# Performance work log

Measured on AMD Instinct MI355X. Metric: run time of the kernel, lower is better.

Reference implementation:

```python
import jax, jax.numpy as jnp
import numpy as np

B, A, G = 16, 32, 512      # batch, atoms, g_feat_in
S, M = 1024, 8             # subset samples, peaks per subset
E, OH = 5, 20              # element types, thermometer size per element
FE = E * OH                # formula encoding = 100
D = 512                    # internal_d
NBINS = 512                # spect bins
EPS = 1e-4


def _ln(x, g, b):
    m = x.mean(-1, keepdims=True)
    v = jnp.mean((x - m) ** 2, -1, keepdims=True)
    return (x - m) * jax.lax.rsqrt(v + 1e-5) * g + b


def setup_inputs() -> dict:
    key = jax.random.key(0)
    ks = jax.random.split(key, 16)
    vert_feat_in = jax.random.normal(ks[0], (B, A, G), jnp.float32)
    vert_mask_in = jnp.ones((B, A), jnp.float32)
    elem = jax.random.randint(ks[1], (B, A), 0, E)
    vert_element_oh = jax.nn.one_hot(elem, E, dtype=jnp.float32)
    atom_subsets = jax.random.randint(ks[2], (B, S, A), 0, 2).astype(jnp.int32)
    atom_subsets_peaks_mass_idx = jax.random.randint(ks[3], (B, S, M), 0, NBINS).astype(jnp.int32)
    atom_subsets_peaks_intensity = jax.random.uniform(ks[4], (B, S, M), jnp.float32)

    def lin(k, o, i):
        s = 1.0 / np.sqrt(i)
        return jax.random.uniform(k, (o, i), jnp.float32, -s, s)

    return dict(
        vert_feat_in=vert_feat_in, vert_mask_in=vert_mask_in,
        vert_element_oh=vert_element_oh, atom_subsets=atom_subsets,
        atom_subsets_peaks_mass_idx=atom_subsets_peaks_mass_idx,
        atom_subsets_peaks_intensity=atom_subsets_peaks_intensity,
        ln_sub_g=jnp.ones((G,)), ln_sub_b=jnp.zeros((G,)),
        W_ih=lin(ks[5], 3 * G, FE), W_hh=lin(ks[6], 3 * G, G),
        b_ih=jnp.zeros((3 * G,)), b_hh=jnp.zeros((3 * G,)),
        ln_post_g=jnp.ones((G,)), ln_post_b=jnp.zeros((G,)),
        W1=lin(ks[7], D, G), b1=jnp.zeros((D,)),
        W2a=lin(ks[8], D, D), b2a=jnp.zeros((D,)),
        W2b=lin(ks[9], D, D), b2b=jnp.zeros((D,)),
        ln_pre_g=jnp.ones((D,)), ln_pre_b=jnp.zeros((D,)),
        W_s=lin(ks[10], 1, D), b_s=jnp.zeros((1,)),
    )


def reference(vert_feat_in, vert_mask_in, vert_element_oh, atom_subsets,
              atom_subsets_peaks_mass_idx, atom_subsets_peaks_intensity,
              ln_sub_g, ln_sub_b, W_ih, W_hh, b_ih, b_hh,
              ln_post_g, ln_post_b, W1, b1, W2a, b2a, W2b, b2b,
              ln_pre_g, ln_pre_b, W_s, b_s):
    subs_f = atom_subsets.astype(jnp.float32)
    masked_vert = vert_feat_in * vert_mask_in[:, :, None]          # B,A,G
    subs_masked = subs_f * vert_mask_in[:, None, :]                 # B,S,A
    # subset-weighted pooling of vertex features
    swv_sum = jnp.einsum('baf,bsa->bsf', masked_vert, subs_masked)  # B,S,G
    subset_size = subs_masked.sum(-1) + EPS                         # B,S
    swv_mean = swv_sum / subset_size[..., None]
    h = _ln(swv_mean, ln_sub_g, ln_sub_b)                           # B,S,G
    # formula counts -> thermometer (accumulating) one-hot; .byte() cast kills grads
    counts = jax.lax.stop_gradient(
        jnp.einsum('bae,bsa->bse', vert_element_oh, subs_f))        # B,S,E
    therm = (jnp.arange(OH, dtype=jnp.float32)[None, None, None, :] < counts[..., None])
    formulae = therm.astype(jnp.float32).reshape(counts.shape[0], counts.shape[1], FE)
    # GRUCell: input=formula encoding, hidden=subset_normed
    gi = jnp.einsum('bsf,gf->bsg', formulae, W_ih) + b_ih           # B,S,3G
    gh = jnp.einsum('bsh,gh->bsg', h, W_hh) + b_hh
    gi_r, gi_z, gi_n = jnp.split(gi, 3, axis=-1)
    gh_r, gh_z, gh_n = jnp.split(gh, 3, axis=-1)
    r = jax.nn.sigmoid(gi_r + gh_r)
    z = jax.nn.sigmoid(gi_z + gh_z)
    n = jnp.tanh(gi_n + r * gh_n)
    combined = (1.0 - z) * n + z * h                                # B,S,G
    x = _ln(combined, ln_post_g, ln_post_b)
    x = jax.nn.relu(jnp.einsum('bsg,dg->bsd', x, W1) + b1)
    x = jax.nn.relu(jnp.einsum('bsd,ed->bse', x, W2a) + b2a)
    x = jax.nn.relu(jnp.einsum('bsd,ed->bse', x, W2b) + b2b)
    x = _ln(x, ln_pre_g, ln_pre_b)
    scores = (jnp.einsum('bsd,od->bso', x, W_s) + b_s)[..., 0]      # B,S
    probs = jax.nn.softmax(scores, axis=-1)                         # B,S
    # sparse mass-matrix multiply: scatter subset probs into spectrum bins
    weighted = atom_subsets_peaks_intensity * probs[:, :, None]     # B,S,M
    bidx = jnp.arange(probs.shape[0])[:, None, None]
    spect_out = jnp.zeros((probs.shape[0], NBINS), probs.dtype)
    spect_out = spect_out.at[bidx, atom_subsets_peaks_mass_idx].add(weighted)
    return spect_out, probs
```

## Files before the change

kernel.cpp:

```cpp
#include <hip/hip_runtime.h>

#define NB 16
#define NA 32
#define NG 512
#define NS 1024
#define NM 8
#define NE 5
#define NOH 20
#define NFE 100
#define NFEP 128
#define ND 512
#define NBINS 512
#define NTOK (NB * NS)

typedef unsigned short ushort_t;
typedef __attribute__((ext_vector_type(8))) short bf16x8;
typedef __attribute__((ext_vector_type(4))) float f32x4;

__device__ __forceinline__ ushort_t f2bf(float x) {
  union { float f; unsigned u; } v; v.f = x;
  unsigned r = v.u + 0x7FFF + ((v.u >> 16) & 1);
  return (ushort_t)(r >> 16);
}
__device__ __forceinline__ float bf2f(ushort_t b) {
  union { unsigned u; float f; } v; v.u = ((unsigned)b) << 16;
  return v.f;
}

__device__ __forceinline__ void gload_lds16(const void* g, void* l) {
  __builtin_amdgcn_global_load_lds(
      (const __attribute__((address_space(1))) void*)g,
      (__attribute__((address_space(3))) void*)l, 16, 0, 0);
}

__device__ inline float breduce256(float v, float* s) {
#pragma unroll
  for (int off = 32; off > 0; off >>= 1) v += __shfl_down(v, off);
  __syncthreads();
  if ((threadIdx.x & 63) == 0) s[threadIdx.x >> 6] = v;
  __syncthreads();
  return s[0] + s[1] + s[2] + s[3];
}

__global__ __launch_bounds__(256) void setup_kernel(
    const float* __restrict__ vert, const float* __restrict__ mask,
    const float* __restrict__ eloh, const int* __restrict__ subs,
    const float* __restrict__ Wih, const float* __restrict__ Whh,
    const float* __restrict__ W1, const float* __restrict__ W2a,
    const float* __restrict__ W2b,
    float* __restrict__ tcd,
    ushort_t* __restrict__ o_ih, ushort_t* __restrict__ o_hh,
    ushort_t* __restrict__ o1, ushort_t* __restrict__ o2a,
    ushort_t* __restrict__ o2b,
    ushort_t* __restrict__ VmT, ushort_t* __restrict__ S_bf) {
  int i = blockIdx.x * 256 + threadIdx.x;
  if (i < NTOK) {
    int b = i >> 10;
    const int* srow = subs + (size_t)i * NA;
    float cnt[NE] = {0.f, 0.f, 0.f, 0.f, 0.f};
    float z = 0.f;
    for (int a = 0; a < NA; a++) {
      float sb = (float)srow[a];
      z += sb * mask[b * NA + a];
      const float* eo = eloh + (size_t)(b * NA + a) * NE;
#pragma unroll
      for (int e = 0; e < NE; e++) cnt[e] += eo[e] * sb;
    }
    float* o = tcd + (size_t)i * 8;
#pragma unroll
    for (int e = 0; e < NE; e++) o[e] = cnt[e];
    o[5] = 1.0f / (z + 1e-4f);
    return;
  }
  i -= NTOK;
  if (i < 1536 * NFEP) {
    int r = i >> 7, c = i & 127;
    o_ih[i] = (c < NFE) ? f2bf(Wih[r * NFE + c]) : (ushort_t)0;
    return;
  }
  i -= 1536 * NFEP;
  if (i < 1536 * NG) { o_hh[i] = f2bf(Whh[i]); return; }
  i -= 1536 * NG;
  if (i < ND * NG) { o1[i] = f2bf(W1[i]); return; }
  i -= ND * NG;
  if (i < ND * ND) { o2a[i] = f2bf(W2a[i]); return; }
  i -= ND * ND;
  if (i < ND * ND) { o2b[i] = f2bf(W2b[i]); return; }
  i -= ND * ND;
  const int nV = NB * NG * NA;
  if (i < nV) {
    int b = i / (NG * NA); int rem = i % (NG * NA);
    int f = rem >> 5, a = rem & 31;
    float mk = mask[b * NA + a];
    VmT[i] = f2bf(vert[(size_t)b * NA * NG + a * NG + f] * mk * mk);
    return;
  }
  i -= nV;
  if (i < NTOK * NA) S_bf[i] = f2bf((float)subs[i]);
}

__global__ __launch_bounds__(256) void pool_gemm(
    const ushort_t* __restrict__ S_bf, const ushort_t* __restrict__ VmT,
    const float* __restrict__ tcd, float* __restrict__ SWV, int tok0) {
  __shared__ ushort_t As[128 * 32];
  __shared__ ushort_t Bs[128 * 32];
  const int t = threadIdx.x;
  const int w = t >> 6, lane = t & 63;
  const int wr = w >> 1, wc = w & 1;
  const int bm = blockIdx.x * 128;
  const int bn = blockIdx.y * 128;
  const int b = (tok0 + bm) >> 10;
  const int srow = lane >> 2, scol = (lane & 3) * 8;
  const ushort_t* Bbase = VmT + (size_t)b * NG * NA;
  gload_lds16(S_bf + (size_t)(tok0 + bm + w * 16 + srow) * 32 + scol, &As[w * 512]);
  gload_lds16(S_bf + (size_t)(tok0 + bm + 64 + w * 16 + srow) * 32 + scol, &As[2048 + w * 512]);
  gload_lds16(Bbase + (size_t)(bn + w * 16 + srow) * 32 + scol, &Bs[w * 512]);
  gload_lds16(Bbase + (size_t)(bn + 64 + w * 16 + srow) * 32 + scol, &Bs[2048 + w * 512]);
  __syncthreads();

  const int lr = lane & 15, lq = lane >> 4;
  f32x4 acc[4][4];
#pragma unroll
  for (int m = 0; m < 4; m++)
#pragma unroll
    for (int n = 0; n < 4; n++) acc[m][n] = (f32x4)0.f;
  bf16x8 a[4], bb[4];
#pragma unroll
  for (int m = 0; m < 4; m++)
    a[m] = *(const bf16x8*)&As[(wr * 64 + m * 16 + lr) * 32 + lq * 8];
#pragma unroll
  for (int n = 0; n < 4; n++)
    bb[n] = *(const bf16x8*)&Bs[(wc * 64 + n * 16 + lr) * 32 + lq * 8];
#pragma unroll
  for (int m = 0; m < 4; m++)
#pragma unroll
    for (int n = 0; n < 4; n++)
      acc[m][n] = __builtin_amdgcn_mfma_f32_16x16x32_bf16(a[m], bb[n], acc[m][n], 0, 0, 0);

#pragma unroll
  for (int n = 0; n < 4; n++) {
    const int col = bn + wc * 64 + n * 16 + lr;
#pragma unroll
    for (int m = 0; m < 4; m++) {
      f32x4 v = acc[m][n];
#pragma unroll
      for (int r = 0; r < 4; r++) {
        int row = bm + wr * 64 + m * 16 + lq * 4 + r;
        float inv = tcd[(size_t)(tok0 + row) * 8 + 5];
        SWV[(size_t)row * NG + col] = v[r] * inv;
      }
    }
  }
}

__global__ __launch_bounds__(256) void finish_kernel(
    const float* __restrict__ SWV, const float* __restrict__ tcd,
    const float* __restrict__ lng, const float* __restrict__ lnb,
    ushort_t* __restrict__ Hb, ushort_t* __restrict__ F, int tok0) {
  const int ltok = blockIdx.x;
  const int token = tok0 + ltok;
  const int t = threadIdx.x;
  __shared__ float s_red[4];
  float2 v = *(const float2*)&SWV[(size_t)ltok * NG + 2 * t];
  float mean = breduce256(v.x + v.y, s_red) * (1.0f / NG);
  float d0 = v.x - mean, d1 = v.y - mean;
  float var = breduce256(d0 * d0 + d1 * d1, s_red) * (1.0f / NG);
  float rstd = rsqrtf(var + 1e-5f);
  float2 g = *(const float2*)&lng[2 * t];
  float2 be = *(const float2*)&lnb[2 * t];
  ushort2 ho;
  ho.x = f2bf(d0 * rstd * g.x + be.x);
  ho.y = f2bf(d1 * rstd * g.y + be.y);
  *(ushort2*)&Hb[(size_t)ltok * NG + 2 * t] = ho;
  if (t < NFEP) {
    float vF = 0.f;
    if (t < NFE) {
      int e = t / NOH, o = t % NOH;
      vF = ((float)o < tcd[(size_t)token * 8 + e]) ? 1.0f : 0.0f;
    }
    F[(size_t)ltok * NFEP + t] = f2bf(vF);
  }
}

__global__ __launch_bounds__(256) void gemm_bf16(
    const ushort_t* __restrict__ A, const ushort_t* __restrict__ W,
    const float* __restrict__ bias, ushort_t* __restrict__ C,
    int K, int Dout, int mode) {
  __shared__ ushort_t As[2][4096];
  __shared__ ushort_t Bs[2][4096];
  const int t = threadIdx.x;
  const int w = t >> 6;
  const int lane = t & 63;
  const int wr = w >> 1, wc = w & 1;
  const int bm = blockIdx.x * 128, bn = blockIdx.y * 128;

  const int srow = lane >> 2;
  const int scol = (lane & 3) * 8;
  const ushort_t* Ag0 = A + (size_t)(bm + w * 16 + srow) * K + scol;
  const ushort_t* Ag1 = A + (size_t)(bm + 64 + w * 16 + srow) * K + scol;
  const ushort_t* Wg0 = W + (size_t)(bn + w * 16 + srow) * K + scol;
  const ushort_t* Wg1 = W + (size_t)(bn + 64 + w * 16 + srow) * K + scol;
  const int l0 = w * 512;
  const int l1 = 2048 + w * 512;

  const int lr = lane & 15;
  const int lq = lane >> 4;

  f32x4 acc[4][4];
#pragma unroll
  for (int m = 0; m < 4; m++)
#pragma unroll
    for (int n = 0; n < 4; n++) acc[m][n] = (f32x4)0.f;

  gload_lds16(Ag0, &As[0][l0]);
  gload_lds16(Ag1, &As[0][l1]);
  gload_lds16(Wg0, &Bs[0][l0]);
  gload_lds16(Wg1, &Bs[0][l1]);
  __syncthreads();

  const int nk = K >> 5;
  int cur = 0;
  for (int kt = 0; kt < nk; kt++) {
    if (kt + 1 < nk) {
      const int k1 = (kt + 1) << 5;
      gload_lds16(Ag0 + k1, &As[cur ^ 1][l0]);
      gload_lds16(Ag1 + k1, &As[cur ^ 1][l1]);
      gload_lds16(Wg0 + k1, &Bs[cur ^ 1][l0]);
      gload_lds16(Wg1 + k1, &Bs[cur ^ 1][l1]);
    }
    bf16x8 a[4], b[4];
#pragma unroll
    for (int m = 0; m < 4; m++)
      a[m] = *(const bf16x8*)&As[cur][(wr * 64 + m * 16 + lr) * 32 + lq * 8];
#pragma unroll
    for (int n = 0; n < 4; n++)
      b[n] = *(const bf16x8*)&Bs[cur][(wc * 64 + n * 16 + lr) * 32 + lq * 8];
#pragma unroll
    for (int m = 0; m < 4; m++)
#pragma unroll
      for (int n = 0; n < 4; n++)
        acc[m][n] = __builtin_amdgcn_mfma_f32_16x16x32_bf16(a[m], b[n], acc[m][n], 0, 0, 0);
    __syncthreads();
    cur ^= 1;
  }

#pragma unroll
  for (int n = 0; n < 4; n++) {
    const int col = bn + wc * 64 + n * 16 + lr;
    const float bv = bias[col];
#pragma unroll
    for (int m = 0; m < 4; m++) {
      f32x4 v = acc[m][n];
#pragma unroll
      for (int r = 0; r < 4; r++) {
        int row = bm + wr * 64 + m * 16 + lq * 4 + r;
        float u = v[r] + bv;
        if (mode == 1) u = fmaxf(u, 0.f);
        C[(size_t)row * Dout + col] = f2bf(u);
      }
    }
  }
}

__global__ __launch_bounds__(256) void gate_ln_kernel(
    const ushort_t* __restrict__ Gi, const ushort_t* __restrict__ Gh,
    const ushort_t* __restrict__ Hb, const float* __restrict__ lng,
    const float* __restrict__ lnb, ushort_t* __restrict__ X0) {
  const int token = blockIdx.x;
  const int t = threadIdx.x;
  __shared__ float s_red[4];
  const ushort_t* gi = Gi + (size_t)token * 1536;
  const ushort_t* gh = Gh + (size_t)token * 1536;
  ushort2 gir = *(const ushort2*)&gi[2 * t];
  ushort2 giz = *(const ushort2*)&gi[NG + 2 * t];
  ushort2 gin = *(const ushort2*)&gi[2 * NG + 2 * t];
  ushort2 ghr = *(const ushort2*)&gh[2 * t];
  ushort2 ghz = *(const ushort2*)&gh[NG + 2 * t];
  ushort2 ghn = *(const ushort2*)&gh[2 * NG + 2 * t];
  ushort2 hh = *(const ushort2*)&Hb[(size_t)token * NG + 2 * t];
  float c[2];
  {
    float r0 = 1.f / (1.f + expf(-(bf2f(gir.x) + bf2f(ghr.x))));
    float z0 = 1.f / (1.f + expf(-(bf2f(giz.x) + bf2f(ghz.x))));
    float n0 = tanhf(bf2f(gin.x) + r0 * bf2f(ghn.x));
    c[0] = (1.f - z0) * n0 + z0 * bf2f(hh.x);
    float r1 = 1.f / (1.f + expf(-(bf2f(gir.y) + bf2f(ghr.y))));
    float z1 = 1.f / (1.f + expf(-(bf2f(giz.y) + bf2f(ghz.y))));
    float n1 = tanhf(bf2f(gin.y) + r1 * bf2f(ghn.y));
    c[1] = (1.f - z1) * n1 + z1 * bf2f(hh.y);
  }
  float mean = breduce256(c[0] + c[1], s_red) * (1.0f / NG);
  float d0 = c[0] - mean, d1 = c[1] - mean;
  float var = breduce256(d0 * d0 + d1 * d1, s_red) * (1.0f / NG);
  float rstd = rsqrtf(var + 1e-5f);
  float2 g = *(const float2*)&lng[2 * t];
  float2 be = *(const float2*)&lnb[2 * t];
  ushort2 xo;
  xo.x = f2bf(d0 * rstd * g.x + be.x);
  xo.y = f2bf(d1 * rstd * g.y + be.y);
  *(ushort2*)&X0[(size_t)token * NG + 2 * t] = xo;
}

__global__ __launch_bounds__(256) void ln_score_kernel(
    const ushort_t* __restrict__ X, const float* __restrict__ lng,
    const float* __restrict__ lnb, const float* __restrict__ Wsc,
    const float* __restrict__ bsc, float* __restrict__ scores) {
  const int token = blockIdx.x;
  const int t = threadIdx.x;
  __shared__ float s_red[4];
  ushort2 xx = *(const ushort2*)&X[(size_t)token * ND + 2 * t];
  float v0 = bf2f(xx.x), v1 = bf2f(xx.y);
  float mean = breduce256(v0 + v1, s_red) * (1.0f / ND);
  float d0 = v0 - mean, d1 = v1 - mean;
  float var = breduce256(d0 * d0 + d1 * d1, s_red) * (1.0f / ND);
  float rstd = rsqrtf(var + 1e-5f);
  float2 g = *(const float2*)&lng[2 * t];
  float2 be = *(const float2*)&lnb[2 * t];
  float2 wv = *(const float2*)&Wsc[2 * t];
  float y0 = d0 * rstd * g.x + be.x;
  float y1 = d1 * rstd * g.y + be.y;
  float dot = breduce256(y0 * wv.x + y1 * wv.y, s_red);
  if (t == 0) scores[token] = dot + bsc[0];
}

__global__ __launch_bounds__(256) void softmax_scatter_kernel(
    const float* __restrict__ scores, const int* __restrict__ pidx,
    const float* __restrict__ pint, float* __restrict__ spect,
    float* __restrict__ probs) {
  const int b = blockIdx.x;
  const int t = threadIdx.x;
  __shared__ float s_red[4];
  __shared__ float s_spec[NBINS];
  const float* sc = scores + (size_t)b * NS;
  float v[4];
  float mx = -1e30f;
#pragma unroll
  for (int i = 0; i < 4; i++) { v[i] = sc[t + i * 256]; mx = fmaxf(mx, v[i]); }
#pragma unroll
  for (int off = 32; off > 0; off >>= 1) mx = fmaxf(mx, __shfl_down(mx, off));
  if ((t & 63) == 0) s_red[t >> 6] = mx;
  __syncthreads();
  mx = fmaxf(fmaxf(s_red[0], s_red[1]), fmaxf(s_red[2], s_red[3]));
  float e[4], sum = 0.f;
#pragma unroll
  for (int i = 0; i < 4; i++) { e[i] = expf(v[i] - mx); sum += e[i]; }
  sum = breduce256(sum, s_red);
  float inv = 1.f / sum;
  s_spec[t] = 0.f; s_spec[t + 256] = 0.f;
  float p[4];
#pragma unroll
  for (int i = 0; i < 4; i++) {
    p[i] = e[i] * inv;
    probs[(size_t)b * NS + t + i * 256] = p[i];
  }
  __syncthreads();
#pragma unroll
  for (int i = 0; i < 4; i++) {
    const int s = t + i * 256;
    const int* idx = pidx + ((size_t)b * NS + s) * NM;
    const float* wt = pint + ((size_t)b * NS + s) * NM;
#pragma unroll
    for (int m = 0; m < NM; m++)
      atomicAdd(&s_spec[idx[m]], wt[m] * p[i]);
  }
  __syncthreads();
  spect[(size_t)b * NBINS + t] = s_spec[t];
  spect[(size_t)b * NBINS + t + 256] = s_spec[t + 256];
}

extern "C" void kernel_launch(void* const* d_in, const int* in_sizes, int n_in,
                              void* d_out, int out_size, void* d_ws, size_t ws_size,
                              hipStream_t stream) {
  const float* vert = (const float*)d_in[0];
  const float* mask = (const float*)d_in[1];
  const float* eloh = (const float*)d_in[2];
  const int* subs = (const int*)d_in[3];
  const int* pidx = (const int*)d_in[4];
  const float* pint = (const float*)d_in[5];
  const float* ln_sub_g = (const float*)d_in[6];
  const float* ln_sub_b = (const float*)d_in[7];
  const float* W_ih = (const float*)d_in[8];
  const float* W_hh = (const float*)d_in[9];
  const float* b_ih = (const float*)d_in[10];
  const float* b_hh = (const float*)d_in[11];
  const float* ln_post_g = (const float*)d_in[12];
  const float* ln_post_b = (const float*)d_in[13];
  const float* W1 = (const float*)d_in[14];
  const float* b1 = (const float*)d_in[15];
  const float* W2a = (const float*)d_in[16];
  const float* b2a = (const float*)d_in[17];
  const float* W2b = (const float*)d_in[18];
  const float* b2b = (const float*)d_in[19];
  const float* ln_pre_g = (const float*)d_in[20];
  const float* ln_pre_b = (const float*)d_in[21];
  const float* W_s = (const float*)d_in[22];
  const float* b_s = (const float*)d_in[23];

  float* out = (float*)d_out;
  float* probs = out + NB * NBINS;

  char* ws = (char*)d_ws;
  float* scores = (float*)ws;
  ushort_t* Wih_bf = (ushort_t*)(ws + 65536);
  ushort_t* Whh_bf = (ushort_t*)(ws + 458752);
  ushort_t* W1_bf  = (ushort_t*)(ws + 2031616);
  ushort_t* W2a_bf = (ushort_t*)(ws + 2555904);
  ushort_t* W2b_bf = (ushort_t*)(ws + 3080192);
  ushort_t* VmT    = (ushort_t*)(ws + 3604480);
  ushort_t* S_bf   = (ushort_t*)(ws + 4128768);
  float*    tcd    = (float*)(ws + 5177344);
  const size_t fixed = 5701632;

  const size_t per_tok = 10496;
  int T = NTOK;
  while (T > 1024 && fixed + (size_t)T * per_tok > ws_size) T >>= 1;
  const int nchunks = NTOK / T;

  char* cb = ws + fixed;
  float*    SWV = (float*)cb;                             cb += (size_t)T * 2048;
  ushort_t* Hb  = (ushort_t*)cb;                          cb += (size_t)T * 1024;
  ushort_t* F   = (ushort_t*)cb;                          cb += (size_t)T * 256;
  ushort_t* Gi  = (ushort_t*)cb;                          cb += (size_t)T * 3072;
  ushort_t* Gh  = (ushort_t*)cb;                          cb += (size_t)T * 3072;
  ushort_t* X0  = (ushort_t*)cb;
  ushort_t* X1  = Gi;
  ushort_t* X2  = Gh;
  ushort_t* X3  = X0;

  const int setup_items = NTOK + 1536 * NFEP + 1536 * NG + 3 * ND * ND
                        + NB * NG * NA + NTOK * NA;
  setup_kernel<<<(setup_items + 255) / 256, 256, 0, stream>>>(
      vert, mask, eloh, subs, W_ih, W_hh, W1, W2a, W2b,
      tcd, Wih_bf, Whh_bf, W1_bf, W2a_bf, W2b_bf, VmT, S_bf);

  for (int c = 0; c < nchunks; c++) {
    const int tok0 = c * T;

    dim3 gp(T / 128, NG / 128);
    pool_gemm<<<gp, 256, 0, stream>>>(S_bf, VmT, tcd, SWV, tok0);
    finish_kernel<<<T, 256, 0, stream>>>(SWV, tcd, ln_sub_g, ln_sub_b, Hb, F, tok0);

    dim3 g1(T / 128, 1536 / 128);
    gemm_bf16<<<g1, 256, 0, stream>>>(F, Wih_bf, b_ih, Gi, NFEP, 1536, 3);
    gemm_bf16<<<g1, 256, 0, stream>>>(Hb, Whh_bf, b_hh, Gh, NG, 1536, 3);

    gate_ln_kernel<<<T, 256, 0, stream>>>(Gi, Gh, Hb, ln_post_g, ln_post_b, X0);

    dim3 g2(T / 128, ND / 128);
    gemm_bf16<<<g2, 256, 0, stream>>>(X0, W1_bf, b1, X1, NG, ND, 1);
    gemm_bf16<<<g2, 256, 0, stream>>>(X1, W2a_bf, b2a, X2, ND, ND, 1);
    gemm_bf16<<<g2, 256, 0, stream>>>(X2, W2b_bf, b2b, X3, ND, ND, 1);

    ln_score_kernel<<<T, 256, 0, stream>>>(X3, ln_pre_g, ln_pre_b, W_s, b_s, scores + tok0);
  }

  softmax_scatter_kernel<<<NB, 256, 0, stream>>>(scores, pidx, pint, out, probs);
}
```

Before: 301.1 us.

## Replace W_ih GEMM with prefix-sum lookup, swizzle LDS, one-wave-per-token norms

The thermometer formula encoding makes W_ih·F a sum of per-element prefix sums of W_ih columns. A prefix-sum table (PS) is now built in setup and gathered in gate_ln, which removes the F matrix, the Gi buffer and one GEMM launch. LDS loads in the GEMMs are XOR-swizzled to cut bank conflicts. The LayerNorm, gate and score kernels now use one wavefront per token with shuffle-only reductions. Gate inputs are computed in fp32 instead of bf16, which changes rounding slightly.

```diff
diff --git a/kernel.cpp b/kernel.cpp
--- a/kernel.cpp
+++ b/kernel.cpp
@@ -8,7 +8,6 @@
 #define NE 5
 #define NOH 20
 #define NFE 100
-#define NFEP 128
 #define ND 512
 #define NBINS 512
 #define NTOK (NB * NS)
@@ -33,13 +32,10 @@
       (__attribute__((address_space(3))) void*)l, 16, 0, 0);
 }
 
-__device__ inline float breduce256(float v, float* s) {
-#pragma unroll
-  for (int off = 32; off > 0; off >>= 1) v += __shfl_down(v, off);
-  __syncthreads();
-  if ((threadIdx.x & 63) == 0) s[threadIdx.x >> 6] = v;
-  __syncthreads();
-  return s[0] + s[1] + s[2] + s[3];
+__device__ __forceinline__ float wsum64(float v) {
+#pragma unroll
+  for (int off = 32; off > 0; off >>= 1) v += __shfl_xor(v, off);
+  return v;
 }
 
 __global__ __launch_bounds__(256) void setup_kernel(
@@ -48,10 +44,9 @@
     const float* __restrict__ Wih, const float* __restrict__ Whh,
     const float* __restrict__ W1, const float* __restrict__ W2a,
     const float* __restrict__ W2b,
-    float* __restrict__ tcd,
-    ushort_t* __restrict__ o_ih, ushort_t* __restrict__ o_hh,
-    ushort_t* __restrict__ o1, ushort_t* __restrict__ o2a,
-    ushort_t* __restrict__ o2b,
+    float* __restrict__ tcd, float* __restrict__ PS,
+    ushort_t* __restrict__ o_hh, ushort_t* __restrict__ o1,
+    ushort_t* __restrict__ o2a, ushort_t* __restrict__ o2b,
     ushort_t* __restrict__ VmT, ushort_t* __restrict__ S_bf) {
   int i = blockIdx.x * 256 + threadIdx.x;
   if (i < NTOK) {
@@ -73,12 +68,18 @@
     return;
   }
   i -= NTOK;
-  if (i < 1536 * NFEP) {
-    int r = i >> 7, c = i & 127;
-    o_ih[i] = (c < NFE) ? f2bf(Wih[r * NFE + c]) : (ushort_t)0;
+  if (i < NE * 1536) {
+    int e = i / 1536, g = i % 1536;
+    float s = 0.f;
+    float* base = PS + ((size_t)e * 21) * 1536 + g;
+    base[0] = 0.f;
+    for (int c = 1; c <= NOH; c++) {
+      s += Wih[(size_t)g * NFE + e * NOH + (c - 1)];
+      base[(size_t)c * 1536] = s;
+    }
     return;
   }
-  i -= 1536 * NFEP;
+  i -= NE * 1536;
   if (i < 1536 * NG) { o_hh[i] = f2bf(Whh[i]); return; }
   i -= 1536 * NG;
   if (i < ND * NG) { o1[i] = f2bf(W1[i]); return; }
@@ -110,7 +111,8 @@
   const int bm = blockIdx.x * 128;
   const int bn = blockIdx.y * 128;
   const int b = (tok0 + bm) >> 10;
-  const int srow = lane >> 2, scol = (lane & 3) * 8;
+  const int srow = lane >> 2;
+  const int scol = (((lane & 3) ^ ((lane >> 3) & 3)) * 8);
   const ushort_t* Bbase = VmT + (size_t)b * NG * NA;
   gload_lds16(S_bf + (size_t)(tok0 + bm + w * 16 + srow) * 32 + scol, &As[w * 512]);
   gload_lds16(S_bf + (size_t)(tok0 + bm + 64 + w * 16 + srow) * 32 + scol, &As[2048 + w * 512]);
@@ -119,6 +121,7 @@
   __syncthreads();
 
   const int lr = lane & 15, lq = lane >> 4;
+  const int rchunk = (lq ^ ((lr >> 1) & 3)) * 8;
   f32x4 acc[4][4];
 #pragma unroll
   for (int m = 0; m < 4; m++)
@@ -127,10 +130,10 @@
   bf16x8 a[4], bb[4];
 #pragma unroll
   for (int m = 0; m < 4; m++)
-    a[m] = *(const bf16x8*)&As[(wr * 64 + m * 16 + lr) * 32 + lq * 8];
+    a[m] = *(const bf16x8*)&As[(wr * 64 + m * 16 + lr) * 32 + rchunk];
 #pragma unroll
   for (int n = 0; n < 4; n++)
-    bb[n] = *(const bf16x8*)&Bs[(wc * 64 + n * 16 + lr) * 32 + lq * 8];
+    bb[n] = *(const bf16x8*)&Bs[(wc * 64 + n * 16 + lr) * 32 + rchunk];
 #pragma unroll
   for (int m = 0; m < 4; m++)
 #pragma unroll
@@ -154,32 +157,32 @@
 }
 
 __global__ __launch_bounds__(256) void finish_kernel(
-    const float* __restrict__ SWV, const float* __restrict__ tcd,
-    const float* __restrict__ lng, const float* __restrict__ lnb,
-    ushort_t* __restrict__ Hb, ushort_t* __restrict__ F, int tok0) {
-  const int ltok = blockIdx.x;
-  const int token = tok0 + ltok;
-  const int t = threadIdx.x;
-  __shared__ float s_red[4];
-  float2 v = *(const float2*)&SWV[(size_t)ltok * NG + 2 * t];
-  float mean = breduce256(v.x + v.y, s_red) * (1.0f / NG);
-  float d0 = v.x - mean, d1 = v.y - mean;
-  float var = breduce256(d0 * d0 + d1 * d1, s_red) * (1.0f / NG);
-  float rstd = rsqrtf(var + 1e-5f);
-  float2 g = *(const float2*)&lng[2 * t];
-  float2 be = *(const float2*)&lnb[2 * t];
-  ushort2 ho;
-  ho.x = f2bf(d0 * rstd * g.x + be.x);
-  ho.y = f2bf(d1 * rstd * g.y + be.y);
-  *(ushort2*)&Hb[(size_t)ltok * NG + 2 * t] = ho;
-  if (t < NFEP) {
-    float vF = 0.f;
-    if (t < NFE) {
-      int e = t / NOH, o = t % NOH;
-      vF = ((float)o < tcd[(size_t)token * 8 + e]) ? 1.0f : 0.0f;
-    }
-    F[(size_t)ltok * NFEP + t] = f2bf(vF);
-  }
+    const float* __restrict__ SWV, const float* __restrict__ lng,
+    const float* __restrict__ lnb, ushort_t* __restrict__ Hb) {
+  const int t = threadIdx.x;
+  const int lane = t & 63, wv = t >> 6;
+  const int ltok = blockIdx.x * 4 + wv;
+  const int f = lane * 8;
+  const float* row = SWV + (size_t)ltok * NG + f;
+  float4 v0 = *(const float4*)row;
+  float4 v1 = *(const float4*)(row + 4);
+  float x[8] = {v0.x, v0.y, v0.z, v0.w, v1.x, v1.y, v1.z, v1.w};
+  float ps = 0.f;
+#pragma unroll
+  for (int j = 0; j < 8; j++) ps += x[j];
+  float mean = wsum64(ps) * (1.0f / NG);
+  float pq = 0.f;
+#pragma unroll
+  for (int j = 0; j < 8; j++) { float d = x[j] - mean; pq += d * d; }
+  float rstd = rsqrtf(wsum64(pq) * (1.0f / NG) + 1e-5f);
+  float4 g0 = *(const float4*)&lng[f], g1 = *(const float4*)&lng[f + 4];
+  float4 b0 = *(const float4*)&lnb[f], b1 = *(const float4*)&lnb[f + 4];
+  float gg[8] = {g0.x, g0.y, g0.z, g0.w, g1.x, g1.y, g1.z, g1.w};
+  float bbv[8] = {b0.x, b0.y, b0.z, b0.w, b1.x, b1.y, b1.z, b1.w};
+  bf16x8 ho;
+#pragma unroll
+  for (int j = 0; j < 8; j++) ho[j] = (short)f2bf((x[j] - mean) * rstd * gg[j] + bbv[j]);
+  *(bf16x8*)&Hb[(size_t)ltok * NG + f] = ho;
 }
 
 __global__ __launch_bounds__(256) void gemm_bf16(
@@ -195,7 +198,7 @@
   const int bm = blockIdx.x * 128, bn = blockIdx.y * 128;
 
   const int srow = lane >> 2;
-  const int scol = (lane & 3) * 8;
+  const int scol = (((lane & 3) ^ ((lane >> 3) & 3)) * 8);
   const ushort_t* Ag0 = A + (size_t)(bm + w * 16 + srow) * K + scol;
   const ushort_t* Ag1 = A + (size_t)(bm + 64 + w * 16 + srow) * K + scol;
   const ushort_t* Wg0 = W + (size_t)(bn + w * 16 + srow) * K + scol;
@@ -205,6 +208,7 @@
 
   const int lr = lane & 15;
   const int lq = lane >> 4;
+  const int rchunk = (lq ^ ((lr >> 1) & 3)) * 8;
 
   f32x4 acc[4][4];
 #pragma unroll
@@ -231,10 +235,10 @@
     bf16x8 a[4], b[4];
 #pragma unroll
     for (int m = 0; m < 4; m++)
-      a[m] = *(const bf16x8*)&As[cur][(wr * 64 + m * 16 + lr) * 32 + lq * 8];
+      a[m] = *(const bf16x8*)&As[cur][(wr * 64 + m * 16 + lr) * 32 + rchunk];
 #pragma unroll
     for (int n = 0; n < 4; n++)
-      b[n] = *(const bf16x8*)&Bs[cur][(wc * 64 + n * 16 + lr) * 32 + lq * 8];
+      b[n] = *(const bf16x8*)&Bs[cur][(wc * 64 + n * 16 + lr) * 32 + rchunk];
 #pragma unroll
     for (int m = 0; m < 4; m++)
 #pragma unroll
@@ -263,64 +267,93 @@
 }
 
 __global__ __launch_bounds__(256) void gate_ln_kernel(
-    const ushort_t* __restrict__ Gi, const ushort_t* __restrict__ Gh,
-    const ushort_t* __restrict__ Hb, const float* __restrict__ lng,
+    const ushort_t* __restrict__ Gh, const ushort_t* __restrict__ Hb,
+    const float* __restrict__ tcd, const float* __restrict__ PS,
+    const float* __restrict__ b_ih, const float* __restrict__ lng,
     const float* __restrict__ lnb, ushort_t* __restrict__ X0) {
-  const int token = blockIdx.x;
-  const int t = threadIdx.x;
-  __shared__ float s_red[4];
-  const ushort_t* gi = Gi + (size_t)token * 1536;
-  const ushort_t* gh = Gh + (size_t)token * 1536;
-  ushort2 gir = *(const ushort2*)&gi[2 * t];
-  ushort2 giz = *(const ushort2*)&gi[NG + 2 * t];
-  ushort2 gin = *(const ushort2*)&gi[2 * NG + 2 * t];
-  ushort2 ghr = *(const ushort2*)&gh[2 * t];
-  ushort2 ghz = *(const ushort2*)&gh[NG + 2 * t];
-  ushort2 ghn = *(const ushort2*)&gh[2 * NG + 2 * t];
-  ushort2 hh = *(const ushort2*)&Hb[(size_t)token * NG + 2 * t];
-  float c[2];
-  {
-    float r0 = 1.f / (1.f + expf(-(bf2f(gir.x) + bf2f(ghr.x))));
-    float z0 = 1.f / (1.f + expf(-(bf2f(giz.x) + bf2f(ghz.x))));
-    float n0 = tanhf(bf2f(gin.x) + r0 * bf2f(ghn.x));
-    c[0] = (1.f - z0) * n0 + z0 * bf2f(hh.x);
-    float r1 = 1.f / (1.f + expf(-(bf2f(gir.y) + bf2f(ghr.y))));
-    float z1 = 1.f / (1.f + expf(-(bf2f(giz.y) + bf2f(ghz.y))));
-    float n1 = tanhf(bf2f(gin.y) + r1 * bf2f(ghn.y));
-    c[1] = (1.f - z1) * n1 + z1 * bf2f(hh.y);
-  }
-  float mean = breduce256(c[0] + c[1], s_red) * (1.0f / NG);
-  float d0 = c[0] - mean, d1 = c[1] - mean;
-  float var = breduce256(d0 * d0 + d1 * d1, s_red) * (1.0f / NG);
-  float rstd = rsqrtf(var + 1e-5f);
-  float2 g = *(const float2*)&lng[2 * t];
-  float2 be = *(const float2*)&lnb[2 * t];
-  ushort2 xo;
-  xo.x = f2bf(d0 * rstd * g.x + be.x);
-  xo.y = f2bf(d1 * rstd * g.y + be.y);
-  *(ushort2*)&X0[(size_t)token * NG + 2 * t] = xo;
+  const int t = threadIdx.x;
+  const int lane = t & 63, wv = t >> 6;
+  const int ltok = blockIdx.x * 4 + wv;
+  const int f = lane * 8;
+  int c[NE];
+#pragma unroll
+  for (int e = 0; e < NE; e++) {
+    int ci = (int)tcd[(size_t)ltok * 8 + e];
+    c[e] = ci > NOH ? NOH : ci;
+  }
+  float4 r0 = *(const float4*)&b_ih[f],          r1 = *(const float4*)&b_ih[f + 4];
+  float4 z0 = *(const float4*)&b_ih[NG + f],     z1 = *(const float4*)&b_ih[NG + f + 4];
+  float4 n0 = *(const float4*)&b_ih[2 * NG + f], n1 = *(const float4*)&b_ih[2 * NG + f + 4];
+#pragma unroll
+  for (int e = 0; e < NE; e++) {
+    const float* pe = PS + ((size_t)(e * 21 + c[e])) * 1536;
+    r0 += *(const float4*)&pe[f];          r1 += *(const float4*)&pe[f + 4];
+    z0 += *(const float4*)&pe[NG + f];     z1 += *(const float4*)&pe[NG + f + 4];
+    n0 += *(const float4*)&pe[2 * NG + f]; n1 += *(const float4*)&pe[2 * NG + f + 4];
+  }
+  float gir[8] = {r0.x, r0.y, r0.z, r0.w, r1.x, r1.y, r1.z, r1.w};
+  float giz[8] = {z0.x, z0.y, z0.z, z0.w, z1.x, z1.y, z1.z, z1.w};
+  float gin[8] = {n0.x, n0.y, n0.z, n0.w, n1.x, n1.y, n1.z, n1.w};
+
+  const ushort_t* gh = Gh + (size_t)ltok * 1536;
+  bf16x8 vr = *(const bf16x8*)&gh[f];
+  bf16x8 vz = *(const bf16x8*)&gh[NG + f];
+  bf16x8 vn = *(const bf16x8*)&gh[2 * NG + f];
+  bf16x8 vh = *(const bf16x8*)&Hb[(size_t)ltok * NG + f];
+  float cv[8];
+  float ps = 0.f;
+#pragma unroll
+  for (int j = 0; j < 8; j++) {
+    float rg = 1.f / (1.f + expf(-(gir[j] + bf2f((ushort_t)vr[j]))));
+    float zg = 1.f / (1.f + expf(-(giz[j] + bf2f((ushort_t)vz[j]))));
+    float ng = tanhf(gin[j] + rg * bf2f((ushort_t)vn[j]));
+    cv[j] = (1.f - zg) * ng + zg * bf2f((ushort_t)vh[j]);
+    ps += cv[j];
+  }
+  float mean = wsum64(ps) * (1.0f / NG);
+  float pq = 0.f;
+#pragma unroll
+  for (int j = 0; j < 8; j++) { float d = cv[j] - mean; pq += d * d; }
+  float rstd = rsqrtf(wsum64(pq) * (1.0f / NG) + 1e-5f);
+  float4 g0 = *(const float4*)&lng[f], g1 = *(const float4*)&lng[f + 4];
+  float4 b0 = *(const float4*)&lnb[f], b1 = *(const float4*)&lnb[f + 4];
+  float gg[8] = {g0.x, g0.y, g0.z, g0.w, g1.x, g1.y, g1.z, g1.w};
+  float bbv[8] = {b0.x, b0.y, b0.z, b0.w, b1.x, b1.y, b1.z, b1.w};
+  bf16x8 xo;
+#pragma unroll
+  for (int j = 0; j < 8; j++) xo[j] = (short)f2bf((cv[j] - mean) * rstd * gg[j] + bbv[j]);
+  *(bf16x8*)&X0[(size_t)ltok * NG + f] = xo;
 }
 
 __global__ __launch_bounds__(256) void ln_score_kernel(
     const ushort_t* __restrict__ X, const float* __restrict__ lng,
     const float* __restrict__ lnb, const float* __restrict__ Wsc,
     const float* __restrict__ bsc, float* __restrict__ scores) {
-  const int token = blockIdx.x;
-  const int t = threadIdx.x;
-  __shared__ float s_red[4];
-  ushort2 xx = *(const ushort2*)&X[(size_t)token * ND + 2 * t];
-  float v0 = bf2f(xx.x), v1 = bf2f(xx.y);
-  float mean = breduce256(v0 + v1, s_red) * (1.0f / ND);
-  float d0 = v0 - mean, d1 = v1 - mean;
-  float var = breduce256(d0 * d0 + d1 * d1, s_red) * (1.0f / ND);
-  float rstd = rsqrtf(var + 1e-5f);
-  float2 g = *(const float2*)&lng[2 * t];
-  float2 be = *(const float2*)&lnb[2 * t];
-  float2 wv = *(const float2*)&Wsc[2 * t];
-  float y0 = d0 * rstd * g.x + be.x;
-  float y1 = d1 * rstd * g.y + be.y;
-  float dot = breduce256(y0 * wv.x + y1 * wv.y, s_red);
-  if (t == 0) scores[token] = dot + bsc[0];
+  const int t = threadIdx.x;
+  const int lane = t & 63, wv = t >> 6;
+  const int ltok = blockIdx.x * 4 + wv;
+  const int f = lane * 8;
+  bf16x8 xx = *(const bf16x8*)&X[(size_t)ltok * ND + f];
+  float x[8];
+  float ps = 0.f;
+#pragma unroll
+  for (int j = 0; j < 8; j++) { x[j] = bf2f((ushort_t)xx[j]); ps += x[j]; }
+  float mean = wsum64(ps) * (1.0f / ND);
+  float pq = 0.f;
+#pragma unroll
+  for (int j = 0; j < 8; j++) { float d = x[j] - mean; pq += d * d; }
+  float rstd = rsqrtf(wsum64(pq) * (1.0f / ND) + 1e-5f);
+  float4 g0 = *(const float4*)&lng[f], g1 = *(const float4*)&lng[f + 4];
+  float4 b0 = *(const float4*)&lnb[f], b1 = *(const float4*)&lnb[f + 4];
+  float4 w0 = *(const float4*)&Wsc[f], w1 = *(const float4*)&Wsc[f + 4];
+  float gg[8] = {g0.x, g0.y, g0.z, g0.w, g1.x, g1.y, g1.z, g1.w};
+  float bbv[8] = {b0.x, b0.y, b0.z, b0.w, b1.x, b1.y, b1.z, b1.w};
+  float ww[8] = {w0.x, w0.y, w0.z, w0.w, w1.x, w1.y, w1.z, w1.w};
+  float d = 0.f;
+#pragma unroll
+  for (int j = 0; j < 8; j++) d += ((x[j] - mean) * rstd * gg[j] + bbv[j]) * ww[j];
+  float dot = wsum64(d);
+  if (lane == 0) scores[ltok] = dot + bsc[0];
 }
 
 __global__ __launch_bounds__(256) void softmax_scatter_kernel(
@@ -344,7 +377,12 @@
   float e[4], sum = 0.f;
 #pragma unroll
   for (int i = 0; i < 4; i++) { e[i] = expf(v[i] - mx); sum += e[i]; }
-  sum = breduce256(sum, s_red);
+#pragma unroll
+  for (int off = 32; off > 0; off >>= 1) sum += __shfl_down(sum, off);
+  __syncthreads();
+  if ((t & 63) == 0) s_red[t >> 6] = sum;
+  __syncthreads();
+  sum = s_red[0] + s_red[1] + s_red[2] + s_red[3];
   float inv = 1.f / sum;
   s_spec[t] = 0.f; s_spec[t + 256] = 0.f;
   float p[4];
@@ -401,17 +439,17 @@
 
   char* ws = (char*)d_ws;
   float* scores = (float*)ws;
-  ushort_t* Wih_bf = (ushort_t*)(ws + 65536);
-  ushort_t* Whh_bf = (ushort_t*)(ws + 458752);
-  ushort_t* W1_bf  = (ushort_t*)(ws + 2031616);
-  ushort_t* W2a_bf = (ushort_t*)(ws + 2555904);
-  ushort_t* W2b_bf = (ushort_t*)(ws + 3080192);
-  ushort_t* VmT    = (ushort_t*)(ws + 3604480);
-  ushort_t* S_bf   = (ushort_t*)(ws + 4128768);
-  float*    tcd    = (float*)(ws + 5177344);
-  const size_t fixed = 5701632;
-
-  const size_t per_tok = 10496;
+  ushort_t* Whh_bf = (ushort_t*)(ws + 65536);
+  ushort_t* W1_bf  = (ushort_t*)(ws + 1638400);
+  ushort_t* W2a_bf = (ushort_t*)(ws + 2162688);
+  ushort_t* W2b_bf = (ushort_t*)(ws + 2686976);
+  ushort_t* VmT    = (ushort_t*)(ws + 3211264);
+  ushort_t* S_bf   = (ushort_t*)(ws + 3735552);
+  float*    tcd    = (float*)(ws + 4784128);
+  float*    PS     = (float*)(ws + 5308416);
+  const size_t fixed = 5953536;
+
+  const size_t per_tok = 7168;
   int T = NTOK;
   while (T > 1024 && fixed + (size_t)T * per_tok > ws_size) T >>= 1;
   const int nchunks = NTOK / T;
@@ -419,39 +457,38 @@
   char* cb = ws + fixed;
   float*    SWV = (float*)cb;                             cb += (size_t)T * 2048;
   ushort_t* Hb  = (ushort_t*)cb;                          cb += (size_t)T * 1024;
-  ushort_t* F   = (ushort_t*)cb;                          cb += (size_t)T * 256;
-  ushort_t* Gi  = (ushort_t*)cb;                          cb += (size_t)T * 3072;
   ushort_t* Gh  = (ushort_t*)cb;                          cb += (size_t)T * 3072;
   ushort_t* X0  = (ushort_t*)cb;
-  ushort_t* X1  = Gi;
-  ushort_t* X2  = Gh;
+  ushort_t* X1  = Gh;
+  ushort_t* X2  = Gh + (size_t)T * 512;
   ushort_t* X3  = X0;
 
-  const int setup_items = NTOK + 1536 * NFEP + 1536 * NG + 3 * ND * ND
+  const int setup_items = NTOK + NE * 1536 + 1536 * NG + ND * NG + 2 * ND * ND
                         + NB * NG * NA + NTOK * NA;
   setup_kernel<<<(setup_items + 255) / 256, 256, 0, stream>>>(
       vert, mask, eloh, subs, W_ih, W_hh, W1, W2a, W2b,
-      tcd, Wih_bf, Whh_bf, W1_bf, W2a_bf, W2b_bf, VmT, S_bf);
+      tcd, PS, Whh_bf, W1_bf, W2a_bf, W2b_bf, VmT, S_bf);
 
   for (int c = 0; c < nchunks; c++) {
     const int tok0 = c * T;
 
     dim3 gp(T / 128, NG / 128);
     pool_gemm<<<gp, 256, 0, stream>>>(S_bf, VmT, tcd, SWV, tok0);
-    finish_kernel<<<T, 256, 0, stream>>>(SWV, tcd, ln_sub_g, ln_sub_b, Hb, F, tok0);
+    finish_kernel<<<T / 4, 256, 0, stream>>>(SWV, ln_sub_g, ln_sub_b, Hb);
 
     dim3 g1(T / 128, 1536 / 128);
-    gemm_bf16<<<g1, 256, 0, stream>>>(F, Wih_bf, b_ih, Gi, NFEP, 1536, 3);
     gemm_bf16<<<g1, 256, 0, stream>>>(Hb, Whh_bf, b_hh, Gh, NG, 1536, 3);
 
-    gate_ln_kernel<<<T, 256, 0, stream>>>(Gi, Gh, Hb, ln_post_g, ln_post_b, X0);
+    gate_ln_kernel<<<T / 4, 256, 0, stream>>>(Gh, Hb, tcd + (size_t)tok0 * 8, PS,
+                                              b_ih, ln_post_g, ln_post_b, X0);
 
     dim3 g2(T / 128, ND / 128);
     gemm_bf16<<<g2, 256, 0, stream>>>(X0, W1_bf, b1, X1, NG, ND, 1);
     gemm_bf16<<<g2, 256, 0, stream>>>(X1, W2a_bf, b2a, X2, ND, ND, 1);
     gemm_bf16<<<g2, 256, 0, stream>>>(X2, W2b_bf, b2b, X3, ND, ND, 1);
 
-    ln_score_kernel<<<T, 256, 0, stream>>>(X3, ln_pre_g, ln_pre_b, W_s, b_s, scores + tok0);
+    ln_score_kernel<<<T / 4, 256, 0, stream>>>(X3, ln_pre_g, ln_pre_b, W_s, b_s,
+                                               scores + tok0);
   }
 
   softmax_scatter_kernel<<<NB, 256, 0, stream>>>(scores, pidx, pint, out, probs);
```

Result: faster. 270.2 us (-10.2%).
